# Optimization experiments

Measured on AMD Instinct MI355X. Metric: run time of the kernel, lower is better.

The kernel has to match this reference:

```python
import jax, jax.numpy as jnp
import numpy as np

TOP_K = 2
CAPACITY_FACTOR = 1.0


def _ffn(x, w1, w2):
    # SwiGLU FFN: x [N, D], w1 [D, 2F], w2 [F, D]
    h = x @ w1
    x1, x2 = jnp.split(h, 2, axis=-1)
    return (x1 * jax.nn.silu(x2)) @ w2


def setup_inputs() -> dict:
    key = jax.random.key(0)
    ks = jax.random.split(key, 6)
    B, S, D, F, E_r, E_s = 4, 2048, 2048, 1024, 7, 1
    sc_in = 1.0 / np.sqrt(D)
    sc_mid = 1.0 / np.sqrt(F)
    return {
        "x": jax.random.normal(ks[0], (B, S, D), dtype=jnp.float32),
        "gate_w": jax.random.normal(ks[1], (D, E_r), dtype=jnp.float32) * sc_in,
        "expert_bias": jnp.zeros((E_r,), dtype=jnp.float32),
        "shared_w1": jax.random.normal(ks[2], (E_s, D, 2 * F), dtype=jnp.float32) * sc_in,
        "shared_w2": jax.random.normal(ks[3], (E_s, F, D), dtype=jnp.float32) * sc_mid,
        "routed_w1": jax.random.normal(ks[4], (E_r, D, 2 * F), dtype=jnp.float32) * sc_in,
        "routed_w2": jax.random.normal(ks[5], (E_r, F, D), dtype=jnp.float32) * sc_mid,
    }


def reference(x, gate_w, expert_bias, shared_w1, shared_w2, routed_w1, routed_w2):
    B, S, D = x.shape
    E_r = gate_w.shape[1]
    T = B * S
    capacity = max(1, int(CAPACITY_FACTOR * T / E_r))
    flat_x = x.reshape(T, D)

    # shared experts: applied to every token, summed
    shared_sum = jax.vmap(_ffn, in_axes=(None, 0, 0))(flat_x, shared_w1, shared_w2).sum(0)

    # gating (eval mode: no noise, no dropout)
    gate_logits = flat_x @ gate_w + expert_bias  # [T, E_r]
    aff = jax.nn.sigmoid(gate_logits)
    _, topk_idx = jax.lax.top_k(aff, TOP_K)  # [T, K]
    # mask[t, e] = expert e is among token t's top-k
    mask = (topk_idx[:, :, None] == jnp.arange(E_r)[None, None, :]).any(axis=1)  # [T, E_r]

    # per-expert capacity selection: keep top-`capacity` masked tokens by affinity
    score = jnp.where(mask, aff, -1.0).T  # [E_r, T]; aff >= 0 so -1 sorts last
    _, sel_idx = jax.lax.top_k(score, capacity)  # [E_r, capacity] token ids
    kept = jnp.take_along_axis(mask.T, sel_idx, axis=1)  # [E_r, cap]
    w = jnp.where(kept, jnp.take_along_axis(aff.T, sel_idx, axis=1), 0.0)  # [E_r, cap]

    # grouped gather -> FFN -> weighted scatter-add
    inp = flat_x[sel_idx]  # [E_r, cap, D]
    out = jax.vmap(_ffn)(inp, routed_w1, routed_w2)  # [E_r, cap, D]
    routed_sum = jnp.zeros_like(flat_x).at[sel_idx].add(out * w[:, :, None])

    return (shared_sum + routed_sum).reshape(B, S, D)
```

## Files before the change

### kernel.cpp

```cpp
#include <hip/hip_runtime.h>
#include <hip/hip_bf16.h>

typedef unsigned long long u64;
typedef __bf16 bf16x8 __attribute__((ext_vector_type(8)));
typedef float f32x4 __attribute__((ext_vector_type(4)));
typedef unsigned short ushort8_t __attribute__((ext_vector_type(8)));

#define TOKS 8192
#define DMODEL 2048
#define FD 1024
#define NEXP 7
#define CAP 1170
#define CAPP 1280

#define MFMA16(a, b, c) __builtin_amdgcn_mfma_f32_16x16x32_bf16(a, b, c, 0, 0, 0)

__device__ __forceinline__ unsigned short f2bf(float f) {
  __hip_bfloat16 b = __float2bfloat16(f);
  return __builtin_bit_cast(unsigned short, b);
}
__device__ __forceinline__ float bf2f(unsigned short u) {
  __hip_bfloat16 b = __builtin_bit_cast(__hip_bfloat16, u);
  return __bfloat162float(b);
}
__device__ __forceinline__ void gload_lds16(const void* g, void* l) {
  __builtin_amdgcn_global_load_lds(
      (const __attribute__((address_space(1))) void*)g,
      (__attribute__((address_space(3))) void*)l, 16, 0, 0);
}

__global__ void k_convert_x(const float* __restrict__ x,
                            unsigned short* __restrict__ xb, long n4) {
  long i = (long)blockIdx.x * blockDim.x + threadIdx.x;
  long stride = (long)gridDim.x * blockDim.x;
  for (; i < n4; i += stride) {
    float4 v = ((const float4*)x)[i];
    ushort4 o;
    o.x = f2bf(v.x); o.y = f2bf(v.y); o.z = f2bf(v.z); o.w = f2bf(v.w);
    ((ushort4*)xb)[i] = o;
  }
}

template <bool PERM>
__global__ void k_transpose_bf16(const float* __restrict__ in0,
                                 const float* __restrict__ inr,
                                 unsigned short* __restrict__ out,
                                 int R, int C) {
  __shared__ float tile[32][33];
  int z = blockIdx.z;
  const float* in = (z == 0) ? in0 : (inr + (long)(z - 1) * R * C);
  unsigned short* o = out + (long)z * R * C;
  int c0 = blockIdx.x * 32;
  int r0 = blockIdx.y * 32;
  int tx = threadIdx.x, ty = threadIdx.y;
#pragma unroll
  for (int k = 0; k < 4; ++k)
    tile[ty + 8 * k][tx] = in[(long)(r0 + ty + 8 * k) * C + c0 + tx];
  __syncthreads();
#pragma unroll
  for (int k = 0; k < 4; ++k) {
    int c = c0 + ty + 8 * k;
    long orow = PERM ? (long)(((c & 1023) >> 4) * 32 + ((c >> 10) << 4) + (c & 15))
                     : (long)c;
    o[orow * R + r0 + tx] = f2bf(tile[tx][ty + 8 * k]);
  }
}

__global__ void k_gating(const float* __restrict__ x,
                         const float* __restrict__ gw,
                         const float* __restrict__ bias,
                         u64* __restrict__ keys) {
  int wave = threadIdx.x >> 6;
  int lane = threadIdx.x & 63;
  int t = blockIdx.x * 4 + wave;
  const float* xr = x + (long)t * DMODEL;
  double acc[NEXP];
#pragma unroll
  for (int e = 0; e < NEXP; ++e) acc[e] = 0.0;
  for (int i = lane; i < DMODEL; i += 64) {
    double xv = (double)xr[i];
    const float* g = gw + (long)i * NEXP;
#pragma unroll
    for (int e = 0; e < NEXP; ++e) acc[e] += xv * (double)g[e];
  }
#pragma unroll
  for (int e = 0; e < NEXP; ++e) {
    for (int off = 32; off > 0; off >>= 1)
      acc[e] += __shfl_down(acc[e], off, 64);
  }
  if (lane == 0) {
    float aff[NEXP];
#pragma unroll
    for (int e = 0; e < NEXP; ++e) {
      double lg = acc[e] + (double)bias[e];
      aff[e] = (float)(1.0 / (1.0 + exp(-lg)));
    }
    int i1 = 0;
    for (int e = 1; e < NEXP; ++e) if (aff[e] > aff[i1]) i1 = e;
    int i2 = -1;
    for (int e = 0; e < NEXP; ++e) {
      if (e == i1) continue;
      if (i2 < 0 || aff[e] > aff[i2]) i2 = e;
    }
#pragma unroll
    for (int e = 0; e < NEXP; ++e) {
      u64 key = (u64)(0xFFFFFFFFu - (unsigned)t);
      if (e == i1 || e == i2) key |= ((u64)__float_as_uint(aff[e])) << 32;
      keys[(long)e * TOKS + t] = key;
    }
  }
}

__global__ __launch_bounds__(1024) void k_sort_select(
    const u64* __restrict__ keys, int* __restrict__ sel,
    float* __restrict__ selw) {
  __shared__ u64 s[TOKS];
  int e = blockIdx.x;
  int tid = threadIdx.x;
  for (int i = tid; i < TOKS; i += 1024) s[i] = keys[(long)e * TOKS + i];
  __syncthreads();
  for (int k = 2; k <= TOKS; k <<= 1) {
    for (int j = k >> 1; j > 0; j >>= 1) {
      for (int ii = tid; ii < TOKS; ii += 1024) {
        int ixj = ii ^ j;
        if (ixj > ii) {
          u64 a = s[ii], b = s[ixj];
          bool descRegion = ((ii & k) == 0);
          bool doSwap = descRegion ? (a < b) : (a > b);
          if (doSwap) { s[ii] = b; s[ixj] = a; }
        }
      }
      __syncthreads();
    }
  }
  for (int i = tid; i < CAPP; i += 1024) {
    u64 key = s[i];
    unsigned vb = (unsigned)(key >> 32);
    int tok = (int)(0xFFFFFFFFu - (unsigned)(key & 0xFFFFFFFFull));
    float w = (i < CAP && vb != 0u) ? __uint_as_float(vb) : 0.0f;
    sel[e * CAPP + i] = tok;
    selw[e * CAPP + i] = w;
  }
}

template <int EPI, bool GATHER>
__global__ __launch_bounds__(512, 2) void k_gemm2ph(
    const unsigned short* __restrict__ Abase,
    const unsigned short* __restrict__ Bbase,
    unsigned short* __restrict__ Cbf, float* __restrict__ Cf32,
    const int* __restrict__ sel, const float* __restrict__ selw,
    int N, int K, long strideA, long strideB, long strideC) {
  extern __shared__ unsigned short lds[];
  const int tid = threadIdx.x;
  const int w = tid >> 6;
  const int lane = tid & 63;

  long lin = blockIdx.x + (long)gridDim.x * (blockIdx.y + (long)gridDim.y * blockIdx.z);
  long nwg = (long)gridDim.x * gridDim.y * gridDim.z;
  long swz = (lin & 7) * (nwg >> 3) + (lin >> 3);
  int bx = (int)(swz % gridDim.x);
  long rem = swz / gridDim.x;
  int by = (int)(rem % gridDim.y);
  int z = (int)(rem / gridDim.y);

  const long m0 = (long)by * 256;
  const long n0 = (long)bx * 256;
  const unsigned short* A = Abase + (GATHER ? 0L : (long)z * strideA);
  const unsigned short* Bm = Bbase + (long)z * strideB;

  const int wr = w >> 2;
  const int wc = w & 3;
  const int lr = lane & 15;
  const int kq = lane >> 4;

  const int srow = (w << 3) + (lane >> 3);
  const int scol = (((lane & 7) ^ (lane >> 3)) << 3);
  const unsigned short* aPtr[4];
  const unsigned short* bPtr[4];
#pragma unroll
  for (int j = 0; j < 4; ++j) {
    int r = j * 64 + srow;
    long ar = GATHER ? (long)sel[z * CAPP + (int)m0 + r] : (m0 + r);
    aPtr[j] = A + ar * (long)K + scol;
    bPtr[j] = Bm + (n0 + r) * (long)K + scol;
  }
  const int dst0 = tid * 8;

  auto STAGE = [&](int buf, int t) {
    unsigned short* base = lds + buf * 32768;
    const long ko = (long)t * 64;
#pragma unroll
    for (int j = 0; j < 4; ++j) {
      gload_lds16(aPtr[j] + ko, base + j * 4096 + dst0);
      gload_lds16(bPtr[j] + ko, base + 16384 + j * 4096 + dst0);
    }
  };

  const int slot0 = (kq ^ (lr & 7)) * 8;
  const int slot1 = ((kq + 4) ^ (lr & 7)) * 8;
  const int aRow = wr * 128 + lr;
  const int bRow = wc * 64 + lr;

  const int nk = K >> 6;

  STAGE(0, 0);
  asm volatile("s_waitcnt vmcnt(0)" ::: "memory");
  __builtin_amdgcn_sched_barrier(0);
  __builtin_amdgcn_s_barrier();
  __builtin_amdgcn_sched_barrier(0);

  f32x4 acc[8][4] = {};
  int cur = 0;

#pragma unroll 1
  for (int t = 0; t < nk; ++t) {
    if (t + 1 < nk) STAGE(cur ^ 1, t + 1);
    const unsigned short* aSeg = lds + cur * 32768;
    const unsigned short* bSeg = aSeg + 16384;
    bf16x8 af[8], bf[4];
#pragma unroll
    for (int m = 0; m < 8; ++m)
      af[m] = *(const bf16x8*)&aSeg[(aRow + m * 16) * 64 + slot0];
#pragma unroll
    for (int n = 0; n < 4; ++n)
      bf[n] = *(const bf16x8*)&bSeg[(bRow + n * 16) * 64 + slot0];
    asm volatile("s_waitcnt lgkmcnt(0)" ::: "memory");
    __builtin_amdgcn_sched_barrier(0);
    __builtin_amdgcn_s_setprio(1);
#pragma unroll
    for (int m = 0; m < 8; ++m)
#pragma unroll
      for (int n = 0; n < 4; ++n)
        acc[m][n] = MFMA16(af[m], bf[n], acc[m][n]);
    __builtin_amdgcn_s_setprio(0);
#pragma unroll
    for (int m = 0; m < 8; ++m)
      af[m] = *(const bf16x8*)&aSeg[(aRow + m * 16) * 64 + slot1];
#pragma unroll
    for (int n = 0; n < 4; ++n)
      bf[n] = *(const bf16x8*)&bSeg[(bRow + n * 16) * 64 + slot1];
    asm volatile("s_waitcnt lgkmcnt(0)" ::: "memory");
    __builtin_amdgcn_sched_barrier(0);
    __builtin_amdgcn_s_setprio(1);
#pragma unroll
    for (int m = 0; m < 8; ++m)
#pragma unroll
      for (int n = 0; n < 4; ++n)
        acc[m][n] = MFMA16(af[m], bf[n], acc[m][n]);
    __builtin_amdgcn_s_setprio(0);
    asm volatile("s_waitcnt vmcnt(0)" ::: "memory");
    __builtin_amdgcn_sched_barrier(0);
    __builtin_amdgcn_s_barrier();
    __builtin_amdgcn_sched_barrier(0);
    cur ^= 1;
  }

  const int r0q = (lane >> 4) * 4;
  const int cc = lane & 15;
  const long crow0 = m0 + wr * 128;
  const long ccol0 = n0 + wc * 64;

  if (EPI == 1) {
#pragma unroll
    for (int m = 0; m < 8; ++m)
#pragma unroll
      for (int r = 0; r < 4; ++r) {
        long row = crow0 + m * 16 + r0q + r;
#pragma unroll
        for (int n = 0; n < 4; ++n)
          Cf32[row * N + ccol0 + n * 16 + cc] = acc[m][n][r];
      }
  } else if (EPI == 2) {
#pragma unroll
    for (int m = 0; m < 8; ++m)
#pragma unroll
      for (int r = 0; r < 4; ++r) {
        int srowi = (int)crow0 + m * 16 + r0q + r;
        int tok = sel[z * CAPP + srowi];
        float wgt = selw[z * CAPP + srowi];
        if (wgt != 0.0f) {
#pragma unroll
          for (int n = 0; n < 4; ++n)
            atomicAdd(&Cf32[(long)tok * N + ccol0 + n * 16 + cc],
                      acc[m][n][r] * wgt);
        }
      }
  } else {
    unsigned short* C = Cbf + (long)z * strideC;
    const int halfN = N >> 1;
    const long gcol0 = (ccol0 >> 1);
#pragma unroll
    for (int m = 0; m < 8; ++m)
#pragma unroll
      for (int r = 0; r < 4; ++r) {
        long row = crow0 + m * 16 + r0q + r;
#pragma unroll
        for (int q = 0; q < 2; ++q) {
          float x1v = acc[m][2 * q][r];
          float x2v = acc[m][2 * q + 1][r];
          float s = x2v / (1.0f + __expf(-x2v));
          C[row * halfN + gcol0 + q * 16 + cc] = f2bf(x1v * s);
        }
      }
  }
}

extern "C" void kernel_launch(void* const* d_in, const int* in_sizes, int n_in,
                              void* d_out, int out_size, void* d_ws,
                              size_t ws_size, hipStream_t stream) {
  (void)in_sizes; (void)n_in; (void)out_size; (void)ws_size;
  const float* x = (const float*)d_in[0];
  const float* gw = (const float*)d_in[1];
  const float* eb = (const float*)d_in[2];
  const float* sw1 = (const float*)d_in[3];
  const float* sw2 = (const float*)d_in[4];
  const float* rw1 = (const float*)d_in[5];
  const float* rw2 = (const float*)d_in[6];
  float* out = (float*)d_out;

  char* ws = (char*)d_ws;
  size_t off = 0;
  auto alloc = [&](size_t bytes) {
    size_t o = off;
    off += (bytes + 255) & ~(size_t)255;
    return o;
  };
  unsigned short* xb  = (unsigned short*)(ws + alloc((size_t)TOKS * DMODEL * 2));
  unsigned short* w1t = (unsigned short*)(ws + alloc((size_t)8 * DMODEL * (2 * FD) * 2));
  unsigned short* w2t = (unsigned short*)(ws + alloc((size_t)8 * DMODEL * FD * 2));
  unsigned short* a_sh = (unsigned short*)(ws + alloc((size_t)TOKS * FD * 2));
  unsigned short* a_r  = (unsigned short*)(ws + alloc((size_t)NEXP * CAPP * FD * 2));
  u64* keys = (u64*)(ws + alloc((size_t)NEXP * TOKS * 8));
  int* sel  = (int*)(ws + alloc((size_t)NEXP * CAPP * 4));
  float* selw = (float*)(ws + alloc((size_t)NEXP * CAPP * 4));

  const size_t LDSB = 131072;

  k_convert_x<<<8192, 256, 0, stream>>>(x, xb, (long)TOKS * DMODEL / 4);
  dim3 tb(32, 8);
  k_transpose_bf16<true><<<dim3(64, 64, 8), tb, 0, stream>>>(sw1, rw1, w1t, DMODEL, 2 * FD);
  k_transpose_bf16<false><<<dim3(64, 32, 8), tb, 0, stream>>>(sw2, rw2, w2t, FD, DMODEL);
  k_gating<<<TOKS / 4, 256, 0, stream>>>(x, gw, eb, keys);
  k_sort_select<<<NEXP, 1024, 0, stream>>>(keys, sel, selw);
  k_gemm2ph<3, false><<<dim3(8, 32, 1), 512, LDSB, stream>>>(
      xb, w1t, a_sh, nullptr, nullptr, nullptr, 2 * FD, DMODEL, 0, 0, 0);
  k_gemm2ph<1, false><<<dim3(8, 32, 1), 512, LDSB, stream>>>(
      a_sh, w2t, nullptr, out, nullptr, nullptr, DMODEL, FD, 0, 0, 0);
  k_gemm2ph<3, true><<<dim3(8, CAPP / 256, NEXP), 512, LDSB, stream>>>(
      xb, w1t + (size_t)DMODEL * (2 * FD), a_r, nullptr, sel, nullptr, 2 * FD,
      DMODEL, 0, (long)DMODEL * (2 * FD), (long)CAPP * FD);
  k_gemm2ph<2, false><<<dim3(8, CAPP / 256, NEXP), 512, LDSB, stream>>>(
      a_r, w2t + (size_t)DMODEL * FD, nullptr, out, sel, selw, DMODEL, FD,
      (long)CAPP * FD, (long)DMODEL * FD, 0);
}
```

Measured before the change: 576.7 us.

## Replace per-expert bitonic sort with radix-select threshold for capacity top-k

Swaps the full 8192-element bitonic sort in shared memory for an 8-pass byte-wise radix select. Each pass builds a 256-bin histogram to find the exact CAP-th largest key, then a final pass compacts every key at or above that threshold using an atomic counter. This removes the many synchronised compare-swap stages of the sort. In exchange the selected tokens land in nondeterministic order, which is acceptable because the later scatter-add does not depend on order, and each pass rereads the keys from global memory.

```diff
diff --git a/kernel.cpp b/kernel.cpp
--- a/kernel.cpp
+++ b/kernel.cpp
@@ -111,35 +111,56 @@
   }
 }
 
-__global__ __launch_bounds__(1024) void k_sort_select(
+__global__ __launch_bounds__(1024) void k_select(
     const u64* __restrict__ keys, int* __restrict__ sel,
     float* __restrict__ selw) {
-  __shared__ u64 s[TOKS];
-  int e = blockIdx.x;
-  int tid = threadIdx.x;
-  for (int i = tid; i < TOKS; i += 1024) s[i] = keys[(long)e * TOKS + i];
+  __shared__ unsigned hist[256];
+  __shared__ u64 s_prefix;
+  __shared__ unsigned s_k;
+  __shared__ unsigned s_cnt;
+  const int e = blockIdx.x;
+  const u64* kk = keys + (long)e * TOKS;
+  const int tid = threadIdx.x;
+  if (tid == 0) { s_prefix = 0; s_k = CAP; s_cnt = 0; }
   __syncthreads();
-  for (int k = 2; k <= TOKS; k <<= 1) {
-    for (int j = k >> 1; j > 0; j >>= 1) {
-      for (int ii = tid; ii < TOKS; ii += 1024) {
-        int ixj = ii ^ j;
-        if (ixj > ii) {
-          u64 a = s[ii], b = s[ixj];
-          bool descRegion = ((ii & k) == 0);
-          bool doSwap = descRegion ? (a < b) : (a > b);
-          if (doSwap) { s[ii] = b; s[ixj] = a; }
+  for (int shift = 56; shift >= 0; shift -= 8) {
+    if (tid < 256) hist[tid] = 0;
+    __syncthreads();
+    u64 pref = s_prefix;
+    for (int i = tid; i < TOKS; i += 1024) {
+      u64 key = kk[i];
+      bool match = (shift == 56) || ((key >> (shift + 8)) == pref);
+      if (match) atomicAdd(&hist[(unsigned)(key >> shift) & 255u], 1u);
+    }
+    __syncthreads();
+    if (tid == 0) {
+      unsigned k = s_k, cum = 0;
+      for (int b = 255; b >= 0; --b) {
+        unsigned c = hist[b];
+        if (cum + c >= k) {
+          s_prefix = (s_prefix << 8) | (unsigned)b;
+          s_k = k - cum;
+          break;
         }
+        cum += c;
       }
-      __syncthreads();
-    }
-  }
-  for (int i = tid; i < CAPP; i += 1024) {
-    u64 key = s[i];
-    unsigned vb = (unsigned)(key >> 32);
-    int tok = (int)(0xFFFFFFFFu - (unsigned)(key & 0xFFFFFFFFull));
-    float w = (i < CAP && vb != 0u) ? __uint_as_float(vb) : 0.0f;
-    sel[e * CAPP + i] = tok;
-    selw[e * CAPP + i] = w;
+    }
+    __syncthreads();
+  }
+  const u64 T = s_prefix;
+  for (int i = tid; i < TOKS; i += 1024) {
+    u64 key = kk[i];
+    if (key >= T) {
+      unsigned p = atomicAdd(&s_cnt, 1u);
+      int tok = (int)(0xFFFFFFFFu - (unsigned)(key & 0xFFFFFFFFull));
+      unsigned vb = (unsigned)(key >> 32);
+      sel[e * CAPP + p] = tok;
+      selw[e * CAPP + p] = vb ? __uint_as_float(vb) : 0.0f;
+    }
+  }
+  for (int i = CAP + tid; i < CAPP; i += 1024) {
+    sel[e * CAPP + i] = 0;
+    selw[e * CAPP + i] = 0.0f;
   }
 }
 
@@ -341,7 +362,7 @@
   k_transpose_bf16<true><<<dim3(64, 64, 8), tb, 0, stream>>>(sw1, rw1, w1t, DMODEL, 2 * FD);
   k_transpose_bf16<false><<<dim3(64, 32, 8), tb, 0, stream>>>(sw2, rw2, w2t, FD, DMODEL);
   k_gating<<<TOKS / 4, 256, 0, stream>>>(x, gw, eb, keys);
-  k_sort_select<<<NEXP, 1024, 0, stream>>>(keys, sel, selw);
+  k_select<<<NEXP, 1024, 0, stream>>>(keys, sel, selw);
   k_gemm2ph<3, false><<<dim3(8, 32, 1), 512, LDSB, stream>>>(
       xb, w1t, a_sh, nullptr, nullptr, nullptr, 2 * FD, DMODEL, 0, 0, 0);
   k_gemm2ph<1, false><<<dim3(8, 32, 1), 512, LDSB, stream>>>(
```

After: 531.2 us. 7.9% less time.
